# Optimization experiments

Hardware: AMD Instinct MI355X
Metric: run time of the kernel (lower is better)

The kernel has to match this reference:

```python
import jax, jax.numpy as jnp
import numpy as np

C = 256  # channels
SHAPES = [(8, C, 80, 80), (8, C, 40, 40), (8, C, 20, 20), (8, C, 10, 10)]
EPS = 1e-8  # torch cosine_similarity eps


def _nearest_resize(x, H, W):
    # Matches F.interpolate(mode='nearest'): src_idx = floor(dst_idx * in/out)
    b, c, h, w = x.shape
    rows = (jnp.arange(H) * h) // H
    cols = (jnp.arange(W) * w) // W
    return x[:, :, rows[:, None], cols[None, :]]


def setup_inputs() -> dict:
    key = jax.random.key(0)
    ks = jax.random.split(key, 12)
    d = {}
    for i, s in enumerate(SHAPES):
        d[f"f{i}"] = jax.random.normal(ks[i], s, dtype=jnp.float32)
        d[f"w{i}"] = jax.random.normal(ks[4 + i], (C, C), dtype=jnp.float32) / jnp.sqrt(jnp.float32(C))
        d[f"b{i}"] = jax.random.normal(ks[8 + i], (C,), dtype=jnp.float32) * 0.01
    return d


def reference(f0, f1, f2, f3, w0, w1, w2, w3, b0, b1, b2, b3):
    feats = [f0, f1, f2, f3]
    ws = [w0, w1, w2, w3]
    bs = [b0, b1, b2, b3]
    H = max(f.shape[2] for f in feats)
    W = max(f.shape[3] for f in feats)
    proj = []
    for f, w, b in zip(feats, ws, bs):
        # 1x1 conv == per-pixel GEMM over channels
        p = jnp.einsum('bchw,oc->bohw', f, w) + b[None, :, None, None]
        if p.shape[2] != H or p.shape[3] != W:
            p = _nearest_resize(p, H, W)
        proj.append(p)
    B = proj[0].shape[0]
    N = len(proj)
    x = jnp.stack(proj, axis=1).reshape(B, N, C, H * W)  # [B,N,C,L]
    # Pairwise cosine similarity along channel dim at each spatial location,
    # then mean over locations (vectorized form of the O(N^2) torch loop).
    dot = jnp.einsum('bicl,bjcl->bijl', x, x)            # [B,N,N,L]
    nrm = jnp.sqrt(jnp.einsum('bicl,bicl->bil', x, x))   # [B,N,L]
    denom = jnp.maximum(nrm[:, :, None, :] * nrm[:, None, :, :], EPS)
    attn = (dot / denom).mean(axis=-1)                   # [B,N,N]
    return jax.nn.softmax(attn, axis=-1)
```

## Files before the change

### kernel.cpp

```cpp
#include <hip/hip_runtime.h>


#define CCH 256
#define WPITCH 40
#define SPITCH 264

typedef __attribute__((ext_vector_type(8))) short short8;
typedef __attribute__((ext_vector_type(4))) short short4_;
typedef __attribute__((ext_vector_type(4))) float float4_;

__device__ inline short f2bf(float x) {
    union { float f; unsigned u; } c; c.f = x;
    unsigned u = c.u + 0x7FFFu + ((c.u >> 16) & 1u);
    return (short)(u >> 16);
}
__device__ inline float bf2f(short b) {
    union { unsigned u; float f; } c; c.u = ((unsigned)(unsigned short)b) << 16;
    return c.f;
}

__device__ inline void dma16(const void* g, void* l) {
    __builtin_amdgcn_global_load_lds(
        (const __attribute__((address_space(1))) void*)g,
        (__attribute__((address_space(3))) void*)l, 16, 0, 0);
}

__global__ __launch_bounds__(256) void proj_small(
    const float* __restrict__ f1, const float* __restrict__ f2,
    const float* __restrict__ f3,
    const float* __restrict__ w0, const float* __restrict__ w1,
    const float* __restrict__ w2, const float* __restrict__ w3,
    const float* __restrict__ b1, const float* __restrict__ b2,
    const float* __restrict__ b3,
    short* __restrict__ u1, short* __restrict__ u2, short* __restrict__ u3,
    short* __restrict__ wp)
{
    __shared__ __align__(16) short Wt[256 * WPITCH];
    __shared__ __align__(16) short Ft[64 * WPITCH];

    const int blk = blockIdx.x;
    const int t = threadIdx.x;

    if (blk >= 272) {
        int id = (blk - 272) * 256 + t;
        int ks = id >> 10;
        int rest = id & 1023;
        int mt = rest >> 6;
        int fl = rest & 63;
        int ln = fl & 15, qd = fl >> 4;
        const float* src = w0 + (size_t)(mt * 16 + ln) * CCH + ks * 32 + qd * 8;
        short8 v;
#pragma unroll
        for (int j = 0; j < 8; ++j) v[j] = f2bf(src[j]);
        *(short8*)(wp + (size_t)id * 8) = v;
        return;
    }

    int b, tile, L;
    const float* F; const float* Wg; const float* bias; short* U;
    if (blk < 200)      { int r = blk;       b = r / 25; tile = r % 25; L = 1600; F = f1; Wg = w1; bias = b1; U = u1; }
    else if (blk < 256) { int r = blk - 200; b = r / 7;  tile = r % 7;  L = 400;  F = f2; Wg = w2; bias = b2; U = u2; }
    else                { int r = blk - 256; b = r / 2;  tile = r % 2;  L = 100;  F = f3; Wg = w3; bias = b3; U = u3; }

    const int lane = t & 63;
    const int wav  = t >> 6;
    const int ln   = lane & 15;
    const int quad = lane >> 4;
    const int pixbase = tile * 64;
    const float* Fb = F + (size_t)b * CCH * L;

    const int wo = t >> 2;
    const int wk = (t & 3) * 8;
    const int fpix = t & 63;
    const int fchunk = t >> 6;
    const int gpix0 = pixbase + fpix;
    const bool pin = gpix0 < L;
    const int gl0 = pin ? gpix0 : 0;

    float4_ wbufA[4], wbufB[4];
    float fbuf[8];
    auto loadW = [&](int ks) {
#pragma unroll
        for (int p = 0; p < 4; ++p) {
            const float* srcp = Wg + (size_t)(p * 64 + wo) * CCH + ks * 32 + wk;
            wbufA[p] = *(const float4_*)srcp;
            wbufB[p] = *(const float4_*)(srcp + 4);
        }
    };
    auto loadF = [&](int ks) {
        const float* fs = Fb + (size_t)(ks * 32 + fchunk * 8) * L + gl0;
#pragma unroll
        for (int j = 0; j < 8; ++j) fbuf[j] = fs[(size_t)j * L];
    };

    float4_ acc[16];
#pragma unroll
    for (int i = 0; i < 16; ++i) acc[i] = (float4_){0.f, 0.f, 0.f, 0.f};

    loadW(0); loadF(0);
    for (int ks = 0; ks < 8; ++ks) {
        __syncthreads();
#pragma unroll
        for (int p = 0; p < 4; ++p) {
            short8 v;
#pragma unroll
            for (int e = 0; e < 4; ++e) { v[e] = f2bf(wbufA[p][e]); v[e + 4] = f2bf(wbufB[p][e]); }
            *(short8*)(&Wt[(p * 64 + wo) * WPITCH + wk]) = v;
        }
        {
            short8 v;
#pragma unroll
            for (int j = 0; j < 8; ++j) v[j] = pin ? f2bf(fbuf[j]) : (short)0;
            *(short8*)(&Ft[fpix * WPITCH + fchunk * 8]) = v;
        }
        __syncthreads();
        const int ksn = (ks + 1) & 7;
        loadW(ksn); loadF(ksn);

        short8 bfrag = *(const short8*)(&Ft[(wav * 16 + ln) * WPITCH + quad * 8]);
#pragma unroll
        for (int mt = 0; mt < 16; ++mt) {
            short8 afrag = *(const short8*)(&Wt[(mt * 16 + ln) * WPITCH + quad * 8]);
            acc[mt] = __builtin_amdgcn_mfma_f32_16x16x32_bf16(afrag, bfrag, acc[mt], 0, 0, 0);
        }
    }

    float ss = 0.f;
#pragma unroll
    for (int mt = 0; mt < 16; ++mt) {
        float4_ bv = *(const float4_*)(bias + mt * 16 + quad * 4);
#pragma unroll
        for (int r = 0; r < 4; ++r) { float v = acc[mt][r] + bv[r]; acc[mt][r] = v; ss += v * v; }
    }
    ss += __shfl_xor(ss, 16);
    ss += __shfl_xor(ss, 32);
    const float inv = 1.f / sqrtf(fmaxf(ss, 1e-24f));

    const int gpixw = pixbase + wav * 16 + ln;
    if (gpixw < L) {
        short* dst = U + ((size_t)b * L + gpixw) * CCH;
#pragma unroll
        for (int mt = 0; mt < 16; ++mt) {
            short4_ v;
#pragma unroll
            for (int r = 0; r < 4; ++r) v[r] = f2bf(acc[mt][r] * inv);
            *(short4_*)(dst + mt * 16 + quad * 4) = v;
        }
    }
}

__global__ __launch_bounds__(512, 2) void proj0_dots(
    const float* __restrict__ F, const short* __restrict__ wp,
    const float* __restrict__ bias,
    const short* __restrict__ u1, const short* __restrict__ u2,
    const short* __restrict__ u3,
    float* __restrict__ partial)
{
    extern __shared__ __align__(16) char smem[];
    short* Wb0 = (short*)smem;
    short* Wb1 = (short*)(smem + 16384);
    float* Fb0 = (float*)(smem + 32768);
    float* Fb1 = (float*)(smem + 65536);
    short* S1 = (short*)smem;
    short* S2 = (short*)(smem + 33792);
    short* S3 = (short*)(smem + 42240);
    float* redF = (float*)(smem + 44352);
    float* redC = (float*)(smem + 44448);

    const int c  = blockIdx.x;
    const int b  = blockIdx.y;
    const int R  = c / 5, C = c - R * 5;
    const int t  = threadIdx.x;
    const int lane = t & 63;
    const int wav  = t >> 6;
    const int ln   = lane & 15;
    const int quad = lane >> 4;
    const float* Fbase = F + (size_t)b * CCH * 6400;

    auto dmaW = [&](int ks, int buf) {
        short* Wb = buf ? Wb1 : Wb0;
#pragma unroll
        for (int m = 0; m < 2; ++m) {
            const int k = wav * 2 + m;
            dma16(wp + (size_t)ks * 8192 + k * 512 + lane * 8, Wb + k * 512);
        }
    };
    auto dmaF = [&](int ks, int buf) {
        float* Fb = buf ? Fb1 : Fb0;
        const int gpx = (16 * R + (lane >> 2)) * 80 + 16 * C + (lane & 3) * 4;
#pragma unroll
        for (int m = 0; m < 4; ++m) {
            const int k = wav * 4 + m;
            dma16(Fbase + (size_t)(ks * 32 + k) * 6400 + gpx, Fb + k * 256);
        }
    };

    float4_ accA[16], accB[16];
#pragma unroll
    for (int i = 0; i < 16; ++i) {
        accA[i] = (float4_){0.f, 0.f, 0.f, 0.f};
        accB[i] = (float4_){0.f, 0.f, 0.f, 0.f};
    }

    const int pxA = wav * 32 + ln;
    const int pxB = pxA + 16;

    dmaW(0, 0); dmaF(0, 0);
    dmaW(1, 1); dmaF(1, 1);
#pragma unroll
    for (int ks = 0; ks < 8; ++ks) {
        if (ks < 7) asm volatile("s_waitcnt vmcnt(6)" ::: "memory");
        else        asm volatile("s_waitcnt vmcnt(0)" ::: "memory");
        __builtin_amdgcn_s_barrier();

        const short* Wl = (ks & 1) ? Wb1 : Wb0;
        const float* Fl = (ks & 1) ? Fb1 : Fb0;
        short8 bfA, bfB;
#pragma unroll
        for (int j = 0; j < 8; ++j) {
            bfA[j] = f2bf(Fl[(quad * 8 + j) * 256 + pxA]);
            bfB[j] = f2bf(Fl[(quad * 8 + j) * 256 + pxB]);
        }
#pragma unroll
        for (int mt = 0; mt < 16; ++mt) {
            short8 afrag = *(const short8*)(Wl + mt * 512 + lane * 8);
            accA[mt] = __builtin_amdgcn_mfma_f32_16x16x32_bf16(afrag, bfA, accA[mt], 0, 0, 0);
            accB[mt] = __builtin_amdgcn_mfma_f32_16x16x32_bf16(afrag, bfB, accB[mt], 0, 0, 0);
        }

        if (ks < 6) {
            asm volatile("s_waitcnt lgkmcnt(0)" ::: "memory");
            __builtin_amdgcn_s_barrier();
            dmaW(ks + 2, ks & 1); dmaF(ks + 2, ks & 1);
        }
    }

    float ssA = 0.f, ssB = 0.f;
#pragma unroll
    for (int mt = 0; mt < 16; ++mt) {
        float4_ bv = *(const float4_*)(bias + mt * 16 + quad * 4);
#pragma unroll
        for (int r = 0; r < 4; ++r) {
            float vA = accA[mt][r] + bv[r]; accA[mt][r] = vA; ssA += vA * vA;
            float vB = accB[mt][r] + bv[r]; accB[mt][r] = vB; ssB += vB * vB;
        }
    }
    ssA += __shfl_xor(ssA, 16); ssA += __shfl_xor(ssA, 32);
    ssB += __shfl_xor(ssB, 16); ssB += __shfl_xor(ssB, 32);
    const float invA = 1.f / sqrtf(fmaxf(ssA, 1e-24f));
    const float invB = 1.f / sqrtf(fmaxf(ssB, 1e-24f));

    __syncthreads();

    {
        const int p1 = t >> 3, co = (t & 7) * 32;
        const int lr = p1 >> 3, lc = p1 & 7;
        const short* src = u1 + ((size_t)(b * 1600 + (8 * R + lr) * 40 + 8 * C + lc)) * CCH + co;
        short* dst = S1 + p1 * SPITCH + co;
#pragma unroll
        for (int j = 0; j < 4; ++j) *(short8*)(dst + j * 8) = *(const short8*)(src + j * 8);
    }
    if (t < 128) {
        const int p2 = t >> 3, co = (t & 7) * 32;
        const int lr = p2 >> 2, lc = p2 & 3;
        const short* src = u2 + ((size_t)(b * 400 + (4 * R + lr) * 20 + 4 * C + lc)) * CCH + co;
        short* dst = S2 + p2 * SPITCH + co;
#pragma unroll
        for (int j = 0; j < 4; ++j) *(short8*)(dst + j * 8) = *(const short8*)(src + j * 8);
    }
    if (t < 32) {
        const int p3 = t >> 3, co = (t & 7) * 32;
        const int lr = p3 >> 1, lc = p3 & 1;
        const short* src = u3 + ((size_t)(b * 100 + (2 * R + lr) * 10 + 2 * C + lc)) * CCH + co;
        short* dst = S3 + p3 * SPITCH + co;
#pragma unroll
        for (int j = 0; j < 4; ++j) *(short8*)(dst + j * 8) = *(const short8*)(src + j * 8);
    }
    __syncthreads();

    const int c1l = wav * 8 + (ln >> 1);
    const int c2l = (wav >> 1) * 4 + (ln >> 2);
    const int c3l = (wav >> 2) * 2 + (ln >> 3);
    float d01 = 0.f, d02 = 0.f, d03 = 0.f;
#pragma unroll
    for (int mt = 0; mt < 16; ++mt) {
        const int ch = mt * 16 + quad * 4;
        short4_ v1 = *(const short4_*)(&S1[c1l * SPITCH + ch]);
        short4_ v2 = *(const short4_*)(&S2[c2l * SPITCH + ch]);
        short4_ v3 = *(const short4_*)(&S3[c3l * SPITCH + ch]);
#pragma unroll
        for (int r = 0; r < 4; ++r) {
            float s = accA[mt][r] * invA + accB[mt][r] * invB;
            d01 += s * bf2f(v1[r]);
            d02 += s * bf2f(v2[r]);
            d03 += s * bf2f(v3[r]);
        }
    }
    {
        float vals[3] = {d01, d02, d03};
#pragma unroll
        for (int p = 0; p < 3; ++p) {
            float v = vals[p];
            v += __shfl_xor(v, 1);  v += __shfl_xor(v, 2);  v += __shfl_xor(v, 4);
            v += __shfl_xor(v, 8);  v += __shfl_xor(v, 16); v += __shfl_xor(v, 32);
            if (lane == 0) redF[wav * 3 + p] = v;
        }
    }

    if (wav < 4) {
        const int p1 = wav * 16 + (lane >> 2);
        const int q  = lane & 3;
        const int lr = p1 >> 3, lc = p1 & 7;
        const int par2 = (lr >> 1) * 4 + (lc >> 1);
        const int par3 = (lr >> 2) * 2 + (lc >> 2);
        float e12 = 0.f, e13 = 0.f;
#pragma unroll
        for (int k = 0; k < 16; ++k) {
            const int co = k * 16 + q * 4;
            short4_ a1 = *(const short4_*)(&S1[p1 * SPITCH + co]);
            short4_ a2 = *(const short4_*)(&S2[par2 * SPITCH + co]);
            short4_ a3 = *(const short4_*)(&S3[par3 * SPITCH + co]);
#pragma unroll
            for (int r = 0; r < 4; ++r) {
                float x1 = bf2f(a1[r]);
                e12 += x1 * bf2f(a2[r]);
                e13 += x1 * bf2f(a3[r]);
            }
        }
        float ev[2] = {e12, e13};
#pragma unroll
        for (int p = 0; p < 2; ++p) {
            float v = ev[p];
            v += __shfl_xor(v, 1);  v += __shfl_xor(v, 2);  v += __shfl_xor(v, 4);
            v += __shfl_xor(v, 8);  v += __shfl_xor(v, 16); v += __shfl_xor(v, 32);
            if (lane == 0) redC[wav * 2 + p] = v;
        }
    } else if (wav == 4) {
        const int p2 = lane >> 2;
        const int q  = lane & 3;
        const int lr = p2 >> 2, lc = p2 & 3;
        const int par3 = (lr >> 1) * 2 + (lc >> 1);
        float e23 = 0.f;
#pragma unroll
        for (int k = 0; k < 16; ++k) {
            const int co = k * 16 + q * 4;
            short4_ a2 = *(const short4_*)(&S2[p2 * SPITCH + co]);
            short4_ a3 = *(const short4_*)(&S3[par3 * SPITCH + co]);
#pragma unroll
            for (int r = 0; r < 4; ++r) e23 += bf2f(a2[r]) * bf2f(a3[r]);
        }
        e23 += __shfl_xor(e23, 1);  e23 += __shfl_xor(e23, 2);  e23 += __shfl_xor(e23, 4);
        e23 += __shfl_xor(e23, 8);  e23 += __shfl_xor(e23, 16); e23 += __shfl_xor(e23, 32);
        if (lane == 0) redC[8] = e23;
    }
    __syncthreads();

    if (t < 6) {
        float v;
        if (t < 3) {
            v = 0.f;
#pragma unroll
            for (int w = 0; w < 8; ++w) v += redF[w * 3 + t];
        } else if (t == 3) v = redC[0] + redC[2] + redC[4] + redC[6];
        else if (t == 4)   v = redC[1] + redC[3] + redC[5] + redC[7];
        else               v = redC[8];
        partial[((size_t)b * 6 + t) * 25 + c] = v;
    }
}

__global__ void softmax4(const float* __restrict__ partial, float* __restrict__ out) {
    int t = threadIdx.x;
    if (t >= 128) return;
    int b = t >> 4, i = (t >> 2) & 3, j = t & 3;
    float a[4];
#pragma unroll
    for (int jj = 0; jj < 4; ++jj) {
        if (jj == i) { a[jj] = 1.0f; continue; }
        int lo = i < jj ? i : jj;
        int hi = i < jj ? jj : i;
        int pidx;
        if (lo == 0) pidx = hi - 1;
        else if (lo == 1) pidx = 1 + hi;
        else pidx = 5;
        const float* pp = partial + ((size_t)b * 6 + pidx) * 25;
        float s = 0.f;
        for (int k = 0; k < 25; ++k) s += pp[k];
        int rf = 80 >> lo;
        a[jj] = s / (float)(rf * rf);
    }
    float m = fmaxf(fmaxf(a[0], a[1]), fmaxf(a[2], a[3]));
    float e0 = expf(a[0] - m), e1 = expf(a[1] - m), e2 = expf(a[2] - m), e3 = expf(a[3] - m);
    float sum = e0 + e1 + e2 + e3;
    float ev = (j == 0) ? e0 : (j == 1) ? e1 : (j == 2) ? e2 : e3;
    out[t] = ev / sum;
}

extern "C" void kernel_launch(void* const* d_in, const int* in_sizes, int n_in,
                              void* d_out, int out_size, void* d_ws, size_t ws_size,
                              hipStream_t stream) {
    const float* f[4]  = {(const float*)d_in[0], (const float*)d_in[3],
                          (const float*)d_in[6], (const float*)d_in[9]};
    const float* w[4]  = {(const float*)d_in[1], (const float*)d_in[4],
                          (const float*)d_in[7], (const float*)d_in[10]};
    const float* bs[4] = {(const float*)d_in[2], (const float*)d_in[5],
                          (const float*)d_in[8], (const float*)d_in[11]};

    char* ws = (char*)d_ws;
    size_t off = 0;
    short* u1 = (short*)(ws + off); off += (size_t)8 * CCH * 1600 * sizeof(short);
    short* u2 = (short*)(ws + off); off += (size_t)8 * CCH * 400  * sizeof(short);
    short* u3 = (short*)(ws + off); off += (size_t)8 * CCH * 100  * sizeof(short);
    short* wp = (short*)(ws + off); off += (size_t)65536 * sizeof(short);
    float* partial = (float*)(ws + off);

    static int smax_set = 0;
    if (!smax_set) {
        hipFuncSetAttribute(reinterpret_cast<const void*>(proj0_dots),
                            hipFuncAttributeMaxDynamicSharedMemorySize, 98304);
        smax_set = 1;
    }

    proj_small<<<304, 256, 0, stream>>>(f[1], f[2], f[3],
                                        w[0], w[1], w[2], w[3],
                                        bs[1], bs[2], bs[3],
                                        u1, u2, u3, wp);

    proj0_dots<<<dim3(25, 8), 512, 98304, stream>>>(f[0], wp, bs[0],
                                                    u1, u2, u3, partial);

    softmax4<<<1, 128, 0, stream>>>(partial, (float*)d_out);
}
```

Measured before the change: 145.9 us.

## Prefetch coarse-level tiles via async LDS DMA alongside GEMM, swizzle layouts

The upsampled-level tiles (u1/u2/u3) are now loaded with global_load_lds DMA at kernel start into dedicated LDS regions. Before, they were copied through registers after the GEMM loop, between two barriers. This overlaps that load with the projection GEMM and removes one sync phase. The F tile DMA and the S tile layouts also get rotation swizzles instead of padding, to avoid LDS bank conflicts. The cost is a larger dynamic LDS footprint (about 138KB), which likely drops occupancy from two blocks per CU to one with 512 threads.

```diff
diff --git a/kernel.cpp b/kernel.cpp
--- a/kernel.cpp
+++ b/kernel.cpp
@@ -3,7 +3,6 @@
 
 #define CCH 256
 #define WPITCH 40
-#define SPITCH 264
 
 typedef __attribute__((ext_vector_type(8))) short short8;
 typedef __attribute__((ext_vector_type(4))) short short4_;
@@ -161,11 +160,11 @@
     short* Wb1 = (short*)(smem + 16384);
     float* Fb0 = (float*)(smem + 32768);
     float* Fb1 = (float*)(smem + 65536);
-    short* S1 = (short*)smem;
-    short* S2 = (short*)(smem + 33792);
-    short* S3 = (short*)(smem + 42240);
-    float* redF = (float*)(smem + 44352);
-    float* redC = (float*)(smem + 44448);
+    short* S1c = (short*)(smem + 98304);
+    short* S2c = (short*)(smem + 131072);
+    short* S3c = (short*)(smem + 139264);
+    float* redF = (float*)(smem + 141312);
+    float* redC = (float*)(smem + 141312 + 96);
 
     const int c  = blockIdx.x;
     const int b  = blockIdx.y;
@@ -187,11 +186,39 @@
     };
     auto dmaF = [&](int ks, int buf) {
         float* Fb = buf ? Fb1 : Fb0;
-        const int gpx = (16 * R + (lane >> 2)) * 80 + 16 * C + (lane & 3) * 4;
 #pragma unroll
         for (int m = 0; m < 4; ++m) {
             const int k = wav * 4 + m;
+            const int p0 = (lane * 4 - (k >> 3) * 8) & 255;
+            const int gpx = (16 * R + (p0 >> 4)) * 80 + 16 * C + (p0 & 15);
             dma16(Fbase + (size_t)(ks * 32 + k) * 6400 + gpx, Fb + k * 256);
+        }
+    };
+    auto dmaU = [&]() {
+#pragma unroll
+        for (int m = 0; m < 4; ++m) {
+            const int Sl = (wav * 4 + m) * 64 + lane;
+            const int px = Sl >> 5;
+            const int so = ((Sl & 31) - px) & 31;
+            const int lr = px >> 3, lc = px & 7;
+            dma16(u1 + ((size_t)(b * 1600 + (8 * R + lr) * 40 + 8 * C + lc)) * CCH + so * 8,
+                  S1c + (wav * 4 + m) * 512);
+        }
+        {
+            const int Sl = wav * 64 + lane;
+            const int px = Sl >> 5;
+            const int so = ((Sl & 31) - px) & 31;
+            const int lr = px >> 2, lc = px & 3;
+            dma16(u2 + ((size_t)(b * 400 + (4 * R + lr) * 20 + 4 * C + lc)) * CCH + so * 8,
+                  S2c + wav * 512);
+        }
+        if (wav < 2) {
+            const int Sl = wav * 64 + lane;
+            const int px = Sl >> 5;
+            const int so = ((Sl & 31) - px) & 31;
+            const int lr = px >> 1, lc = px & 1;
+            dma16(u3 + ((size_t)(b * 100 + (2 * R + lr) * 10 + 2 * C + lc)) * CCH + so * 8,
+                  S3c + wav * 512);
         }
     };
 
@@ -204,7 +231,10 @@
 
     const int pxA = wav * 32 + ln;
     const int pxB = pxA + 16;
-
+    const int rotA = (pxA + 8 * quad) & 255;
+    const int rotB = (pxB + 8 * quad) & 255;
+
+    dmaU();
     dmaW(0, 0); dmaF(0, 0);
     dmaW(1, 1); dmaF(1, 1);
 #pragma unroll
@@ -218,8 +248,8 @@
         short8 bfA, bfB;
 #pragma unroll
         for (int j = 0; j < 8; ++j) {
-            bfA[j] = f2bf(Fl[(quad * 8 + j) * 256 + pxA]);
-            bfB[j] = f2bf(Fl[(quad * 8 + j) * 256 + pxB]);
+            bfA[j] = f2bf(Fl[(quad * 8 + j) * 256 + rotA]);
+            bfB[j] = f2bf(Fl[(quad * 8 + j) * 256 + rotB]);
         }
 #pragma unroll
         for (int mt = 0; mt < 16; ++mt) {
@@ -250,44 +280,17 @@
     const float invA = 1.f / sqrtf(fmaxf(ssA, 1e-24f));
     const float invB = 1.f / sqrtf(fmaxf(ssB, 1e-24f));
 
-    __syncthreads();
-
-    {
-        const int p1 = t >> 3, co = (t & 7) * 32;
-        const int lr = p1 >> 3, lc = p1 & 7;
-        const short* src = u1 + ((size_t)(b * 1600 + (8 * R + lr) * 40 + 8 * C + lc)) * CCH + co;
-        short* dst = S1 + p1 * SPITCH + co;
-#pragma unroll
-        for (int j = 0; j < 4; ++j) *(short8*)(dst + j * 8) = *(const short8*)(src + j * 8);
-    }
-    if (t < 128) {
-        const int p2 = t >> 3, co = (t & 7) * 32;
-        const int lr = p2 >> 2, lc = p2 & 3;
-        const short* src = u2 + ((size_t)(b * 400 + (4 * R + lr) * 20 + 4 * C + lc)) * CCH + co;
-        short* dst = S2 + p2 * SPITCH + co;
-#pragma unroll
-        for (int j = 0; j < 4; ++j) *(short8*)(dst + j * 8) = *(const short8*)(src + j * 8);
-    }
-    if (t < 32) {
-        const int p3 = t >> 3, co = (t & 7) * 32;
-        const int lr = p3 >> 1, lc = p3 & 1;
-        const short* src = u3 + ((size_t)(b * 100 + (2 * R + lr) * 10 + 2 * C + lc)) * CCH + co;
-        short* dst = S3 + p3 * SPITCH + co;
-#pragma unroll
-        for (int j = 0; j < 4; ++j) *(short8*)(dst + j * 8) = *(const short8*)(src + j * 8);
-    }
-    __syncthreads();
-
     const int c1l = wav * 8 + (ln >> 1);
     const int c2l = (wav >> 1) * 4 + (ln >> 2);
     const int c3l = (wav >> 2) * 2 + (ln >> 3);
     float d01 = 0.f, d02 = 0.f, d03 = 0.f;
 #pragma unroll
     for (int mt = 0; mt < 16; ++mt) {
-        const int ch = mt * 16 + quad * 4;
-        short4_ v1 = *(const short4_*)(&S1[c1l * SPITCH + ch]);
-        short4_ v2 = *(const short4_*)(&S2[c2l * SPITCH + ch]);
-        short4_ v3 = *(const short4_*)(&S3[c3l * SPITCH + ch]);
+        const int so = 2 * mt + (quad >> 1);
+        const int hf = (quad & 1) * 4;
+        short4_ v1 = *(const short4_*)(&S1c[c1l * 256 + ((so + c1l) & 31) * 8 + hf]);
+        short4_ v2 = *(const short4_*)(&S2c[c2l * 256 + ((so + c2l) & 31) * 8 + hf]);
+        short4_ v3 = *(const short4_*)(&S3c[c3l * 256 + ((so + c3l) & 31) * 8 + hf]);
 #pragma unroll
         for (int r = 0; r < 4; ++r) {
             float s = accA[mt][r] * invA + accB[mt][r] * invB;
@@ -316,10 +319,11 @@
         float e12 = 0.f, e13 = 0.f;
 #pragma unroll
         for (int k = 0; k < 16; ++k) {
-            const int co = k * 16 + q * 4;
-            short4_ a1 = *(const short4_*)(&S1[p1 * SPITCH + co]);
-            short4_ a2 = *(const short4_*)(&S2[par2 * SPITCH + co]);
-            short4_ a3 = *(const short4_*)(&S3[par3 * SPITCH + co]);
+            const int so = 2 * k + (q >> 1);
+            const int hf = (q & 1) * 4;
+            short4_ a1 = *(const short4_*)(&S1c[p1 * 256 + ((so + p1) & 31) * 8 + hf]);
+            short4_ a2 = *(const short4_*)(&S2c[par2 * 256 + ((so + par2) & 31) * 8 + hf]);
+            short4_ a3 = *(const short4_*)(&S3c[par3 * 256 + ((so + par3) & 31) * 8 + hf]);
 #pragma unroll
             for (int r = 0; r < 4; ++r) {
                 float x1 = bf2f(a1[r]);
@@ -343,9 +347,10 @@
         float e23 = 0.f;
 #pragma unroll
         for (int k = 0; k < 16; ++k) {
-            const int co = k * 16 + q * 4;
-            short4_ a2 = *(const short4_*)(&S2[p2 * SPITCH + co]);
-            short4_ a3 = *(const short4_*)(&S3[par3 * SPITCH + co]);
+            const int so = 2 * k + (q >> 1);
+            const int hf = (q & 1) * 4;
+            short4_ a2 = *(const short4_*)(&S2c[p2 * 256 + ((so + p2) & 31) * 8 + hf]);
+            short4_ a3 = *(const short4_*)(&S3c[par3 * 256 + ((so + par3) & 31) * 8 + hf]);
 #pragma unroll
             for (int r = 0; r < 4; ++r) e23 += bf2f(a2[r]) * bf2f(a3[r]);
         }
@@ -416,7 +421,7 @@
     static int smax_set = 0;
     if (!smax_set) {
         hipFuncSetAttribute(reinterpret_cast<const void*>(proj0_dots),
-                            hipFuncAttributeMaxDynamicSharedMemorySize, 98304);
+                            hipFuncAttributeMaxDynamicSharedMemorySize, 141568);
         smax_set = 1;
     }
 
@@ -425,8 +430,8 @@
                                         bs[1], bs[2], bs[3],
                                         u1, u2, u3, wp);
 
-    proj0_dots<<<dim3(25, 8), 512, 98304, stream>>>(f[0], wp, bs[0],
-                                                    u1, u2, u3, partial);
+    proj0_dots<<<dim3(25, 8), 512, 141568, stream>>>(f[0], wp, bs[0],
+                                                     u1, u2, u3, partial);
 
     softmax4<<<1, 128, 0, stream>>>(partial, (float*)d_out);
 }
```

Measured after the change: 147.2 us. Within noise of the previous version (+0.9%).

## Pre-pack all weights to bf16 and DMA-pipeline proj_small loads into LDS

Applied to the files above, without the earlier changes.

Adds a separate pack_w kernel that converts all four weight matrices into MFMA-fragment-ordered bf16 once per call. proj_small then no longer converts weights per block: it uses global_load_lds DMA with double-buffered LDS for both packed weights and fp32 features, and converts features to bf16 at fragment read time. This removes redundant fp32→bf16 conversion and register-staged loads, in exchange for an extra kernel launch. It also relies on clamped pixel addresses for partial tiles.

```diff
diff --git a/kernel.cpp b/kernel.cpp
--- a/kernel.cpp
+++ b/kernel.cpp
@@ -2,8 +2,6 @@
 
 
 #define CCH 256
-#define WPITCH 40
-#define SPITCH 264
 
 typedef __attribute__((ext_vector_type(8))) short short8;
 typedef __attribute__((ext_vector_type(4))) short short4_;
@@ -25,42 +23,47 @@
         (__attribute__((address_space(3))) void*)l, 16, 0, 0);
 }
 
+__global__ __launch_bounds__(256) void pack_w(
+    const float* __restrict__ w0, const float* __restrict__ w1,
+    const float* __restrict__ w2, const float* __restrict__ w3,
+    short* __restrict__ wp)
+{
+    int id = blockIdx.x * 256 + threadIdx.x;
+    int mtx = id >> 13;
+    const float* w = (mtx == 0) ? w0 : (mtx == 1) ? w1 : (mtx == 2) ? w2 : w3;
+    int rest = id & 8191;
+    int ks = rest >> 10;
+    int r2 = rest & 1023;
+    int mt = r2 >> 6;
+    int fl = r2 & 63;
+    int ln = fl & 15, qd = fl >> 4;
+    const float* src = w + (size_t)(mt * 16 + ln) * CCH + ks * 32 + qd * 8;
+    short8 v;
+#pragma unroll
+    for (int j = 0; j < 8; ++j) v[j] = f2bf(src[j]);
+    *(short8*)(wp + (size_t)id * 8) = v;
+}
+
 __global__ __launch_bounds__(256) void proj_small(
     const float* __restrict__ f1, const float* __restrict__ f2,
-    const float* __restrict__ f3,
-    const float* __restrict__ w0, const float* __restrict__ w1,
-    const float* __restrict__ w2, const float* __restrict__ w3,
+    const float* __restrict__ f3, const short* __restrict__ wp,
     const float* __restrict__ b1, const float* __restrict__ b2,
     const float* __restrict__ b3,
-    short* __restrict__ u1, short* __restrict__ u2, short* __restrict__ u3,
-    short* __restrict__ wp)
+    short* __restrict__ u1, short* __restrict__ u2, short* __restrict__ u3)
 {
-    __shared__ __align__(16) short Wt[256 * WPITCH];
-    __shared__ __align__(16) short Ft[64 * WPITCH];
+    __shared__ __align__(16) short Wt0[16 * 512];
+    __shared__ __align__(16) short Wt1[16 * 512];
+    __shared__ __align__(16) float Ft0[32 * 64];
+    __shared__ __align__(16) float Ft1[32 * 64];
 
     const int blk = blockIdx.x;
     const int t = threadIdx.x;
 
-    if (blk >= 272) {
-        int id = (blk - 272) * 256 + t;
-        int ks = id >> 10;
-        int rest = id & 1023;
-        int mt = rest >> 6;
-        int fl = rest & 63;
-        int ln = fl & 15, qd = fl >> 4;
-        const float* src = w0 + (size_t)(mt * 16 + ln) * CCH + ks * 32 + qd * 8;
-        short8 v;
-#pragma unroll
-        for (int j = 0; j < 8; ++j) v[j] = f2bf(src[j]);
-        *(short8*)(wp + (size_t)id * 8) = v;
-        return;
-    }
-
-    int b, tile, L;
-    const float* F; const float* Wg; const float* bias; short* U;
-    if (blk < 200)      { int r = blk;       b = r / 25; tile = r % 25; L = 1600; F = f1; Wg = w1; bias = b1; U = u1; }
-    else if (blk < 256) { int r = blk - 200; b = r / 7;  tile = r % 7;  L = 400;  F = f2; Wg = w2; bias = b2; U = u2; }
-    else                { int r = blk - 256; b = r / 2;  tile = r % 2;  L = 100;  F = f3; Wg = w3; bias = b3; U = u3; }
+    int b, tile, L, sidx;
+    const float* F; const float* bias; short* U;
+    if (blk < 200)      { int r = blk;       b = r / 25; tile = r % 25; L = 1600; F = f1; bias = b1; U = u1; sidx = 1; }
+    else if (blk < 256) { int r = blk - 200; b = r / 7;  tile = r % 7;  L = 400;  F = f2; bias = b2; U = u2; sidx = 2; }
+    else                { int r = blk - 256; b = r / 2;  tile = r % 2;  L = 100;  F = f3; bias = b3; U = u3; sidx = 3; }
 
     const int lane = t & 63;
     const int wav  = t >> 6;
@@ -68,60 +71,60 @@
     const int quad = lane >> 4;
     const int pixbase = tile * 64;
     const float* Fb = F + (size_t)b * CCH * L;
-
-    const int wo = t >> 2;
-    const int wk = (t & 3) * 8;
-    const int fpix = t & 63;
-    const int fchunk = t >> 6;
-    const int gpix0 = pixbase + fpix;
-    const bool pin = gpix0 < L;
-    const int gl0 = pin ? gpix0 : 0;
-
-    float4_ wbufA[4], wbufB[4];
-    float fbuf[8];
-    auto loadW = [&](int ks) {
-#pragma unroll
-        for (int p = 0; p < 4; ++p) {
-            const float* srcp = Wg + (size_t)(p * 64 + wo) * CCH + ks * 32 + wk;
-            wbufA[p] = *(const float4_*)srcp;
-            wbufB[p] = *(const float4_*)(srcp + 4);
+    const short* wps = wp + (size_t)sidx * 65536;
+
+    int gp = pixbase + (lane & 15) * 4;
+    if (gp > L - 4) gp = L - 4;
+    const int chq = lane >> 4;
+
+    auto dmaW = [&](int ks, int buf) {
+        short* Wb = buf ? Wt1 : Wt0;
+#pragma unroll
+        for (int m = 0; m < 4; ++m) {
+            const int k = wav * 4 + m;
+            dma16(wps + (size_t)ks * 8192 + k * 512 + lane * 8, Wb + k * 512);
         }
     };
-    auto loadF = [&](int ks) {
-        const float* fs = Fb + (size_t)(ks * 32 + fchunk * 8) * L + gl0;
-#pragma unroll
-        for (int j = 0; j < 8; ++j) fbuf[j] = fs[(size_t)j * L];
+    auto dmaF = [&](int ks, int buf) {
+        float* Fb_l = buf ? Ft1 : Ft0;
+#pragma unroll
+        for (int m = 0; m < 2; ++m) {
+            const int k4 = wav * 2 + m;
+            const int ch = k4 * 4 + chq;
+            dma16(Fb + (size_t)(ks * 32 + ch) * L + gp, Fb_l + k4 * 256);
+        }
     };
 
     float4_ acc[16];
 #pragma unroll
     for (int i = 0; i < 16; ++i) acc[i] = (float4_){0.f, 0.f, 0.f, 0.f};
 
-    loadW(0); loadF(0);
+    const int fpx = wav * 16 + ln;
+
+    dmaW(0, 0); dmaF(0, 0);
+    dmaW(1, 1); dmaF(1, 1);
+#pragma unroll
     for (int ks = 0; ks < 8; ++ks) {
-        __syncthreads();
-#pragma unroll
-        for (int p = 0; p < 4; ++p) {
-            short8 v;
-#pragma unroll
-            for (int e = 0; e < 4; ++e) { v[e] = f2bf(wbufA[p][e]); v[e + 4] = f2bf(wbufB[p][e]); }
-            *(short8*)(&Wt[(p * 64 + wo) * WPITCH + wk]) = v;
-        }
-        {
-            short8 v;
-#pragma unroll
-            for (int j = 0; j < 8; ++j) v[j] = pin ? f2bf(fbuf[j]) : (short)0;
-            *(short8*)(&Ft[fpix * WPITCH + fchunk * 8]) = v;
-        }
-        __syncthreads();
-        const int ksn = (ks + 1) & 7;
-        loadW(ksn); loadF(ksn);
-
-        short8 bfrag = *(const short8*)(&Ft[(wav * 16 + ln) * WPITCH + quad * 8]);
+        if (ks < 7) asm volatile("s_waitcnt vmcnt(6)" ::: "memory");
+        else        asm volatile("s_waitcnt vmcnt(0)" ::: "memory");
+        __builtin_amdgcn_s_barrier();
+
+        const short* Wl = (ks & 1) ? Wt1 : Wt0;
+        const float* Fl = (ks & 1) ? Ft1 : Ft0;
+        short8 bfrag;
+#pragma unroll
+        for (int j = 0; j < 8; ++j)
+            bfrag[j] = f2bf(Fl[(quad * 8 + j) * 64 + fpx]);
 #pragma unroll
         for (int mt = 0; mt < 16; ++mt) {
-            short8 afrag = *(const short8*)(&Wt[(mt * 16 + ln) * WPITCH + quad * 8]);
+            short8 afrag = *(const short8*)(Wl + mt * 512 + lane * 8);
             acc[mt] = __builtin_amdgcn_mfma_f32_16x16x32_bf16(afrag, bfrag, acc[mt], 0, 0, 0);
+        }
+
+        if (ks < 6) {
+            asm volatile("s_waitcnt lgkmcnt(0)" ::: "memory");
+            __builtin_amdgcn_s_barrier();
+            dmaW(ks + 2, ks & 1); dmaF(ks + 2, ks & 1);
         }
     }
 
@@ -136,7 +139,7 @@
     ss += __shfl_xor(ss, 32);
     const float inv = 1.f / sqrtf(fmaxf(ss, 1e-24f));
 
-    const int gpixw = pixbase + wav * 16 + ln;
+    const int gpixw = pixbase + fpx;
     if (gpixw < L) {
         short* dst = U + ((size_t)b * L + gpixw) * CCH;
 #pragma unroll
@@ -149,6 +152,7 @@
     }
 }
 
+#define SPITCH 264
 __global__ __launch_bounds__(512, 2) void proj0_dots(
     const float* __restrict__ F, const short* __restrict__ wp,
     const float* __restrict__ bias,
@@ -410,7 +414,7 @@
     short* u1 = (short*)(ws + off); off += (size_t)8 * CCH * 1600 * sizeof(short);
     short* u2 = (short*)(ws + off); off += (size_t)8 * CCH * 400  * sizeof(short);
     short* u3 = (short*)(ws + off); off += (size_t)8 * CCH * 100  * sizeof(short);
-    short* wp = (short*)(ws + off); off += (size_t)65536 * sizeof(short);
+    short* wp = (short*)(ws + off); off += (size_t)4 * 65536 * sizeof(short);
     float* partial = (float*)(ws + off);
 
     static int smax_set = 0;
@@ -420,10 +424,11 @@
         smax_set = 1;
     }
 
-    proj_small<<<304, 256, 0, stream>>>(f[1], f[2], f[3],
-                                        w[0], w[1], w[2], w[3],
+    pack_w<<<128, 256, 0, stream>>>(w[0], w[1], w[2], w[3], wp);
+
+    proj_small<<<272, 256, 0, stream>>>(f[1], f[2], f[3], wp,
                                         bs[1], bs[2], bs[3],
-                                        u1, u2, u3, wp);
+                                        u1, u2, u3);
 
     proj0_dots<<<dim3(25, 8), 512, 98304, stream>>>(f[0], wp, bs[0],
                                                     u1, u2, u3, partial);
```

Measured after the change: 143.0 us, median of 3. 1.02x faster.
